# Performance work log

Measured on AMD Instinct MI355X. Metric: run time of the kernel, lower is better.

## Reference

```python
import jax, jax.numpy as jnp
import numpy as np

DT = 0.1
NUM_STEPS = 10
THRESHOLD = 0.3


def setup_inputs() -> dict:
    key = jax.random.key(0)
    k1, k2, k3 = jax.random.split(key, 3)
    B, T, D = 8, 4096, 1024
    L, O = 3, 4
    x = jax.random.normal(k1, (B, T, D), dtype=jnp.float32)
    # nn.Linear(dim, O, bias=False) weights per level, stacked: (L, O, D)
    W = jax.random.normal(k2, (L, O, D), dtype=jnp.float32) / np.sqrt(D)
    # omegas init: randn*0.1 + freq_scales[min(i,2)], freq_scales=[4.0,2.0,0.6]
    freq = jnp.array([4.0, 2.0, 0.6], dtype=jnp.float32)[:, None]
    omegas = jax.random.normal(k3, (L, O), dtype=jnp.float32) * 0.1 + freq
    # coupling strengths: 1.0 + i*0.5
    Ks = 1.0 + 0.5 * jnp.arange(L, dtype=jnp.float32)
    return {"x": x, "W": W, "omegas": omegas, "Ks": Ks}


def reference(x, W, omegas, Ks):
    B, T, D = x.shape
    L, O, _ = W.shape
    two_pi = 2.0 * jnp.pi

    # per-level projection: (L, B, T, O)
    proj = jnp.einsum('btd,lod->lbto', x, W)
    # initial phases from adjacent oscillator ratio
    phases = jnp.arctan2(proj, jnp.roll(proj, 1, axis=-1) + 1e-8) % two_pi

    om = omegas[:, None, None, :]      # (L,1,1,O)
    K = Ks[:, None, None, None]        # (L,1,1,1)

    def step(ph, _):
        # mean phase over time dim per oscillator (circular mean)
        mean_phase = jnp.arctan2(jnp.sin(ph).mean(axis=2, keepdims=True),
                                 jnp.cos(ph).mean(axis=2, keepdims=True))
        coupling = K * jnp.sin(mean_phase - ph) / T
        return (ph + DT * (om + coupling)) % two_pi, None

    phases, _ = jax.lax.scan(step, phases, None, length=NUM_STEPS)

    s = jnp.sin(phases)
    c = jnp.cos(phases)
    # global coherence: |mean_t exp(i*phi)| averaged over oscillators -> (B, L)
    level_coherences = jnp.sqrt(s.mean(axis=2) ** 2 + c.mean(axis=2) ** 2).mean(-1).T

    # sliding window-of-3 coherence along T -> (L, B, T-2)
    ms = (s[:, :, :-2] + s[:, :, 1:-1] + s[:, :, 2:]) / 3.0
    mc = (c[:, :, :-2] + c[:, :, 1:-1] + c[:, :, 2:]) / 3.0
    coh = jnp.sqrt(ms ** 2 + mc ** 2).mean(-1)
    # local-minimum dip detection: boundary at coherence index i+1 (i in 1..T-5)
    cond = (coh[..., 1:-1] < coh[..., :-2] - THRESHOLD) & \
           (coh[..., 1:-1] < coh[..., 2:] - THRESHOLD)      # (L, B, T-4)
    boundary_mask = jnp.pad(cond, ((0, 0), (0, 0), (2, 0)))   # (L, B, T-2)

    return phases, level_coherences, boundary_mask
```

## Files before the change

kernel.cpp:

```cpp
#include <hip/hip_runtime.h>
#include <math.h>

#define NB 8
#define NT 4096
#define ND 1024
#define NL 3
#define NO 4
#define NLO 12
#define TWO_PI_D 6.283185307179586476925286766559
#define DT_D 0.1
#define NSTEPS 10
#define THRESH_D 0.3

#define XPAD 132

__global__ __launch_bounds__(256) void k_wprep(const float* __restrict__ W,
                                               double* __restrict__ wsW)
{
    int i = blockIdx.x * 256 + threadIdx.x;
    if (i < NLO * ND) wsW[i] = (double)W[i];
}

__global__ __launch_bounds__(256, 2) void k_proj(
    const float* __restrict__ x, const double* __restrict__ wsW,
    double* __restrict__ ws_ph, double* __restrict__ ws_s,
    double* __restrict__ ws_c)
{
    __shared__ float  xl[64 * XPAD];
    __shared__ double wl[NLO * 128];
    __shared__ double red[4 * 16 * 4 * 13];

    const int tid = threadIdx.x;
    const int rowslot = tid & 15;
    const int seg = tid >> 4;
    const long row0 = (long)blockIdx.x * 64;

    double acc[4][NLO];
#pragma unroll
    for (int j = 0; j < 4; ++j)
#pragma unroll
        for (int lo = 0; lo < NLO; ++lo) acc[j][lo] = 0.0;

    for (int c = 0; c < ND / 128; ++c) {
#pragma unroll
        for (int p = 0; p < 8; ++p) {
            int id = p * 256 + tid;
            int r = id >> 5, col = id & 31;
            float4 v = *reinterpret_cast<const float4*>(
                x + (row0 + r) * ND + c * 128 + col * 4);
            *reinterpret_cast<float4*>(&xl[r * XPAD + col * 4]) = v;
        }
#pragma unroll
        for (int p = 0; p < 3; ++p) {
            int id = p * 256 + tid;
            int lo = id >> 6, dc = id & 63;
            double2 v = *reinterpret_cast<const double2*>(
                wsW + lo * ND + c * 128 + dc * 2);
            *reinterpret_cast<double2*>(&wl[lo * 128 + dc * 2]) = v;
        }
        __syncthreads();

        const int d0 = seg * 8;
        float xs[4][8];
#pragma unroll
        for (int j = 0; j < 4; ++j) {
            const float* xr = &xl[(rowslot * 4 + j) * XPAD + d0];
            float4 a = *reinterpret_cast<const float4*>(xr);
            float4 b = *reinterpret_cast<const float4*>(xr + 4);
            xs[j][0] = a.x; xs[j][1] = a.y; xs[j][2] = a.z; xs[j][3] = a.w;
            xs[j][4] = b.x; xs[j][5] = b.y; xs[j][6] = b.z; xs[j][7] = b.w;
        }
#pragma unroll
        for (int dp = 0; dp < 4; ++dp) {
            double2 wv[NLO];
#pragma unroll
            for (int lo = 0; lo < NLO; ++lo)
                wv[lo] = *reinterpret_cast<const double2*>(
                    &wl[lo * 128 + d0 + dp * 2]);
#pragma unroll
            for (int j = 0; j < 4; ++j) {
                double x0 = (double)xs[j][2 * dp];
                double x1 = (double)xs[j][2 * dp + 1];
#pragma unroll
                for (int lo = 0; lo < NLO; ++lo)
                    acc[j][lo] = fma(x1, wv[lo].y, fma(x0, wv[lo].x, acc[j][lo]));
            }
        }
        __syncthreads();
    }

#pragma unroll
    for (int j = 0; j < 4; ++j)
#pragma unroll
        for (int lo = 0; lo < NLO; ++lo) {
            double v = acc[j][lo];
            v += __shfl_xor(v, 16, 64);
            v += __shfl_xor(v, 32, 64);
            acc[j][lo] = v;
        }
    const int wv_ = tid >> 6;
    if ((tid & 63) < 16) {
#pragma unroll
        for (int j = 0; j < 4; ++j)
#pragma unroll
            for (int lo = 0; lo < NLO; ++lo)
                red[((wv_ * 16 + rowslot) * 4 + j) * 13 + lo] = acc[j][lo];
    }
    __syncthreads();

    if (tid < 64) {
        const int rs = tid >> 2, j = tid & 3;
        double proj[NLO];
#pragma unroll
        for (int lo = 0; lo < NLO; ++lo)
            proj[lo] = (red[((rs) * 4 + j) * 13 + lo] +
                        red[((16 + rs) * 4 + j) * 13 + lo]) +
                       (red[((32 + rs) * 4 + j) * 13 + lo] +
                        red[((48 + rs) * 4 + j) * 13 + lo]);
        const long row = row0 + tid;
        const int b = (int)(row >> 12);
        const int t = (int)(row & (NT - 1));
#pragma unroll
        for (int l = 0; l < NL; ++l)
#pragma unroll
            for (int o = 0; o < NO; ++o) {
                double y = proj[l * NO + o];
                double xx = proj[l * NO + ((o + 3) & 3)] + 1e-8;
                double ph = atan2(y, xx);
                if (ph < 0.0) ph += TWO_PI_D;
                double r2 = sqrt(y * y + xx * xx);
                double s, cc;
                if (r2 > 0.0) { s = y / r2; cc = xx / r2; } else { s = 0.0; cc = 1.0; }
                long idx = ((long)((l * NB + b) * NO + o)) * NT + t;
                ws_ph[idx] = ph; ws_s[idx] = s; ws_c[idx] = cc;
            }
    }
}

#define B_THREADS 512
#define B_ELEMS (NT / B_THREADS)

__global__ __launch_bounds__(B_THREADS) void k_kuramoto(
    const float* __restrict__ omegas, const float* __restrict__ Ks,
    double* __restrict__ ws_ph, double* __restrict__ ws_s,
    double* __restrict__ ws_c, double* __restrict__ ws_r,
    float* __restrict__ out_ph)
{
    const int g = blockIdx.x;
    const int l = g >> 5;
    const int b = (g >> 2) & 7;
    const int o = g & 3;
    const double om = (double)omegas[l * NO + o];
    const double Kv = (double)Ks[l];
    const int tid = threadIdx.x;
    const int wid = tid >> 6;
    const int lane = tid & 63;
    __shared__ double lds[18];

    double ph[B_ELEMS], s[B_ELEMS], c[B_ELEMS];
#pragma unroll
    for (int k = 0; k < B_ELEMS; ++k) {
        long idx = (long)g * NT + tid + k * B_THREADS;
        ph[k] = ws_ph[idx]; s[k] = ws_s[idx]; c[k] = ws_c[idx];
    }

    for (int step = 0; step < NSTEPS; ++step) {
        double ts = 0.0, tc = 0.0;
#pragma unroll
        for (int k = 0; k < B_ELEMS; ++k) { ts += s[k]; tc += c[k]; }
#pragma unroll
        for (int off = 32; off > 0; off >>= 1) {
            ts += __shfl_down(ts, off);
            tc += __shfl_down(tc, off);
        }
        if (lane == 0) { lds[wid] = ts; lds[8 + wid] = tc; }
        __syncthreads();
        if (tid == 0) {
            double S = 0.0, C = 0.0;
#pragma unroll
            for (int w = 0; w < 8; ++w) { S += lds[w]; C += lds[8 + w]; }
            double mean = atan2(S / (double)NT, C / (double)NT);
            double sm, cm; sincos(mean, &sm, &cm);
            lds[16] = sm; lds[17] = cm;
        }
        __syncthreads();
        const double sm = lds[16], cm = lds[17];
#pragma unroll
        for (int k = 0; k < B_ELEMS; ++k) {
            double sv = sm * c[k] - cm * s[k];
            double d = DT_D * (om + Kv * sv / (double)NT);
            double val = ph[k] + d;
            if (val >= TWO_PI_D) val -= TWO_PI_D;
            if (val < 0.0) val += TWO_PI_D;
            ph[k] = val;
            double z = d * d;
            double sd = d * fma(z, fma(z, fma(z, fma(z, 1.0 / 362880.0,
                          -1.0 / 5040.0), 1.0 / 120.0), -1.0 / 6.0), 1.0);
            double cd = fma(z, fma(z, fma(z, fma(z, 1.0 / 40320.0,
                          -1.0 / 720.0), 1.0 / 24.0), -0.5), 1.0);
            double sn = fma(s[k], cd, c[k] * sd);
            double cn = fma(c[k], cd, -(s[k] * sd));
            s[k] = sn; c[k] = cn;
        }
        __syncthreads();
    }
    {
        double ts = 0.0, tc = 0.0;
#pragma unroll
        for (int k = 0; k < B_ELEMS; ++k) { ts += s[k]; tc += c[k]; }
#pragma unroll
        for (int off = 32; off > 0; off >>= 1) {
            ts += __shfl_down(ts, off);
            tc += __shfl_down(tc, off);
        }
        if (lane == 0) { lds[wid] = ts; lds[8 + wid] = tc; }
        __syncthreads();
        if (tid == 0) {
            double S = 0.0, C = 0.0;
#pragma unroll
            for (int w = 0; w < 8; ++w) { S += lds[w]; C += lds[8 + w]; }
            double Sm = S / (double)NT, Cm = C / (double)NT;
            ws_r[g] = sqrt(Sm * Sm + Cm * Cm);
        }
    }
#pragma unroll
    for (int k = 0; k < B_ELEMS; ++k) {
        int t = tid + k * B_THREADS;
        long idx = (long)g * NT + t;
        ws_s[idx] = s[k]; ws_c[idx] = c[k];
        out_ph[((long)(l * NB + b) * NT + t) * NO + o] = (float)ph[k];
    }
}

__global__ __launch_bounds__(256) void k_mask(
    const double* __restrict__ ws_s, const double* __restrict__ ws_c,
    float* __restrict__ out_mask)
{
    const int bid = blockIdx.x;
    const int lb = bid >> 4;
    const int t0 = ((bid & 15) << 8) + threadIdx.x;
    float* mrow = out_mask + (long)lb * (NT - 2);
    if ((bid & 15) == 0 && threadIdx.x < 2) mrow[threadIdx.x] = 0.0f;
    if (t0 >= NT - 4) return;
    double q[3] = {0.0, 0.0, 0.0};
#pragma unroll
    for (int o = 0; o < NO; ++o) {
        const double* ps = ws_s + ((long)lb * NO + o) * NT + t0;
        const double* pc = ws_c + ((long)lb * NO + o) * NT + t0;
        double sv[5], cv[5];
#pragma unroll
        for (int j = 0; j < 5; ++j) { sv[j] = ps[j]; cv[j] = pc[j]; }
#pragma unroll
        for (int j = 0; j < 3; ++j) {
            double ms = ((sv[j] + sv[j + 1]) + sv[j + 2]) / 3.0;
            double mc = ((cv[j] + cv[j + 1]) + cv[j + 2]) / 3.0;
            q[j] += sqrt(ms * ms + mc * mc);
        }
    }
    double coh0 = q[0] / 4.0, coh1 = q[1] / 4.0, coh2 = q[2] / 4.0;
    bool cond = (coh1 < coh0 - THRESH_D) && (coh1 < coh2 - THRESH_D);
    mrow[2 + t0] = cond ? 1.0f : 0.0f;
}

__global__ void k_level(const double* __restrict__ ws_r, float* __restrict__ out_lvl)
{
    const int tid = threadIdx.x;
    if (tid < NB * NL) {
        const int b = tid / NL, l = tid % NL;
        const double* r = ws_r + (long)(l * NB + b) * NO;
        double m = (((r[0] + r[1]) + r[2]) + r[3]) / 4.0;
        out_lvl[tid] = (float)m;
    }
}

extern "C" void kernel_launch(void* const* d_in, const int* in_sizes, int n_in,
                              void* d_out, int out_size, void* d_ws, size_t ws_size,
                              hipStream_t stream)
{
    const float* x      = (const float*)d_in[0];
    const float* W      = (const float*)d_in[1];
    const float* omegas = (const float*)d_in[2];
    const float* Ks     = (const float*)d_in[3];
    float* out = (float*)d_out;

    double* wsW   = (double*)d_ws;
    double* ws_ph = wsW + NLO * ND;
    double* ws_s  = ws_ph + (long)NLO * NB * NT;
    double* ws_c  = ws_s + (long)NLO * NB * NT;
    double* ws_r  = ws_c + (long)NLO * NB * NT;

    float* out_ph   = out;
    float* out_lvl  = out + 393216;
    float* out_mask = out + 393240;

    k_wprep<<<(NLO * ND + 255) / 256, 256, 0, stream>>>(W, wsW);
    k_proj<<<NB * NT / 64, 256, 0, stream>>>(x, wsW, ws_ph, ws_s, ws_c);
    k_kuramoto<<<NL * NB * NO, B_THREADS, 0, stream>>>(omegas, Ks, ws_ph, ws_s, ws_c, ws_r, out_ph);
    k_mask<<<24 * 16, 256, 0, stream>>>(ws_s, ws_c, out_mask);
    k_level<<<1, 64, 0, stream>>>(ws_r, out_lvl);
}
```

Baseline: 79.75 us.

## Rework projection to per-row direct loads and simplify Kuramoto phase-rotation math

The projection kernel drops LDS staging of x and W. Each thread now owns one row and a 256-wide slice of D, reading x and the double weights straight from global memory into 32 doubles of registers, with a cross-wave reduction through shared memory afterwards. The Kuramoto step replaces atan2+sincos with a normalisation of (S,C). It also replaces the per-element Taylor polynomial for sin/cos of the phase increment with a precomputed sincos(dt*omega) plus a first-order correction in the small coupling term. The first-order correction is an approximation that drops terms of order eps squared, and the new projection relies on cache hits for the weights and raises register pressure.

```diff
diff --git a/kernel.cpp b/kernel.cpp
--- a/kernel.cpp
+++ b/kernel.cpp
@@ -12,8 +12,6 @@
 #define NSTEPS 10
 #define THRESH_D 0.3
 
-#define XPAD 132
-
 __global__ __launch_bounds__(256) void k_wprep(const float* __restrict__ W,
                                                double* __restrict__ wsW)
 {
@@ -21,105 +19,63 @@
     if (i < NLO * ND) wsW[i] = (double)W[i];
 }
 
-__global__ __launch_bounds__(256, 2) void k_proj(
+__global__ __launch_bounds__(256) void k_proj(
     const float* __restrict__ x, const double* __restrict__ wsW,
     double* __restrict__ ws_ph, double* __restrict__ ws_s,
     double* __restrict__ ws_c)
 {
-    __shared__ float  xl[64 * XPAD];
-    __shared__ double wl[NLO * 128];
-    __shared__ double red[4 * 16 * 4 * 13];
-
+    __shared__ double red[4 * 64 * 13];
     const int tid = threadIdx.x;
-    const int rowslot = tid & 15;
-    const int seg = tid >> 4;
-    const long row0 = (long)blockIdx.x * 64;
-
-    double acc[4][NLO];
-#pragma unroll
-    for (int j = 0; j < 4; ++j)
-#pragma unroll
-        for (int lo = 0; lo < NLO; ++lo) acc[j][lo] = 0.0;
-
-    for (int c = 0; c < ND / 128; ++c) {
-#pragma unroll
-        for (int p = 0; p < 8; ++p) {
-            int id = p * 256 + tid;
-            int r = id >> 5, col = id & 31;
-            float4 v = *reinterpret_cast<const float4*>(
-                x + (row0 + r) * ND + c * 128 + col * 4);
-            *reinterpret_cast<float4*>(&xl[r * XPAD + col * 4]) = v;
-        }
-#pragma unroll
-        for (int p = 0; p < 3; ++p) {
-            int id = p * 256 + tid;
-            int lo = id >> 6, dc = id & 63;
-            double2 v = *reinterpret_cast<const double2*>(
-                wsW + lo * ND + c * 128 + dc * 2);
-            *reinterpret_cast<double2*>(&wl[lo * 128 + dc * 2]) = v;
-        }
-        __syncthreads();
-
-        const int d0 = seg * 8;
-        float xs[4][8];
-#pragma unroll
-        for (int j = 0; j < 4; ++j) {
-            const float* xr = &xl[(rowslot * 4 + j) * XPAD + d0];
-            float4 a = *reinterpret_cast<const float4*>(xr);
-            float4 b = *reinterpret_cast<const float4*>(xr + 4);
-            xs[j][0] = a.x; xs[j][1] = a.y; xs[j][2] = a.z; xs[j][3] = a.w;
-            xs[j][4] = b.x; xs[j][5] = b.y; xs[j][6] = b.z; xs[j][7] = b.w;
-        }
-#pragma unroll
-        for (int dp = 0; dp < 4; ++dp) {
-            double2 wv[NLO];
-#pragma unroll
-            for (int lo = 0; lo < NLO; ++lo)
-                wv[lo] = *reinterpret_cast<const double2*>(
-                    &wl[lo * 128 + d0 + dp * 2]);
-#pragma unroll
-            for (int j = 0; j < 4; ++j) {
-                double x0 = (double)xs[j][2 * dp];
-                double x1 = (double)xs[j][2 * dp + 1];
-#pragma unroll
-                for (int lo = 0; lo < NLO; ++lo)
-                    acc[j][lo] = fma(x1, wv[lo].y, fma(x0, wv[lo].x, acc[j][lo]));
-            }
-        }
-        __syncthreads();
-    }
-
-#pragma unroll
-    for (int j = 0; j < 4; ++j)
+    const int lane = tid & 63;
+    const int wid = tid >> 6;
+    const long row = (long)blockIdx.x * 64 + lane;
+    const float* xr = x + row * ND + wid * 256;
+
+    double acc[NLO];
+#pragma unroll
+    for (int lo = 0; lo < NLO; ++lo) acc[lo] = 0.0;
+
+    for (int it = 0; it < 8; ++it) {
+        float4 f[8];
+#pragma unroll
+        for (int q = 0; q < 8; ++q)
+            f[q] = reinterpret_cast<const float4*>(xr + it * 32)[q];
+        double xd[32];
+#pragma unroll
+        for (int q = 0; q < 8; ++q) {
+            xd[q * 4 + 0] = (double)f[q].x;
+            xd[q * 4 + 1] = (double)f[q].y;
+            xd[q * 4 + 2] = (double)f[q].z;
+            xd[q * 4 + 3] = (double)f[q].w;
+        }
+        const double* wp = wsW + wid * 256 + it * 32;
 #pragma unroll
         for (int lo = 0; lo < NLO; ++lo) {
-            double v = acc[j][lo];
-            v += __shfl_xor(v, 16, 64);
-            v += __shfl_xor(v, 32, 64);
-            acc[j][lo] = v;
-        }
-    const int wv_ = tid >> 6;
-    if ((tid & 63) < 16) {
-#pragma unroll
-        for (int j = 0; j < 4; ++j)
-#pragma unroll
-            for (int lo = 0; lo < NLO; ++lo)
-                red[((wv_ * 16 + rowslot) * 4 + j) * 13 + lo] = acc[j][lo];
-    }
+            const double* w = wp + lo * ND;
+            double a = acc[lo];
+#pragma unroll
+            for (int q = 0; q < 32; ++q)
+                a = fma(xd[q], w[q], a);
+            acc[lo] = a;
+        }
+    }
+
+#pragma unroll
+    for (int lo = 0; lo < NLO; ++lo)
+        red[(wid * 64 + lane) * 13 + lo] = acc[lo];
     __syncthreads();
 
     if (tid < 64) {
-        const int rs = tid >> 2, j = tid & 3;
         double proj[NLO];
 #pragma unroll
         for (int lo = 0; lo < NLO; ++lo)
-            proj[lo] = (red[((rs) * 4 + j) * 13 + lo] +
-                        red[((16 + rs) * 4 + j) * 13 + lo]) +
-                       (red[((32 + rs) * 4 + j) * 13 + lo] +
-                        red[((48 + rs) * 4 + j) * 13 + lo]);
-        const long row = row0 + tid;
-        const int b = (int)(row >> 12);
-        const int t = (int)(row & (NT - 1));
+            proj[lo] = (red[(0 * 64 + tid) * 13 + lo] +
+                        red[(1 * 64 + tid) * 13 + lo]) +
+                       (red[(2 * 64 + tid) * 13 + lo] +
+                        red[(3 * 64 + tid) * 13 + lo]);
+        const long r = (long)blockIdx.x * 64 + tid;
+        const int b = (int)(r >> 12);
+        const int t = (int)(r & (NT - 1));
 #pragma unroll
         for (int l = 0; l < NL; ++l)
 #pragma unroll
@@ -152,6 +108,9 @@
     const int o = g & 3;
     const double om = (double)omegas[l * NO + o];
     const double Kv = (double)Ks[l];
+    const double dtom = DT_D * om;
+    const double cKT = DT_D * Kv / (double)NT;
+    double sA, cA; sincos(dtom, &sA, &cA);
     const int tid = threadIdx.x;
     const int wid = tid >> 6;
     const int lane = tid & 63;
@@ -179,8 +138,9 @@
             double S = 0.0, C = 0.0;
 #pragma unroll
             for (int w = 0; w < 8; ++w) { S += lds[w]; C += lds[8 + w]; }
-            double mean = atan2(S / (double)NT, C / (double)NT);
-            double sm, cm; sincos(mean, &sm, &cm);
+            double r2 = sqrt(S * S + C * C);
+            double sm, cm;
+            if (r2 > 0.0) { sm = S / r2; cm = C / r2; } else { sm = 0.0; cm = 1.0; }
             lds[16] = sm; lds[17] = cm;
         }
         __syncthreads();
@@ -188,16 +148,13 @@
 #pragma unroll
         for (int k = 0; k < B_ELEMS; ++k) {
             double sv = sm * c[k] - cm * s[k];
-            double d = DT_D * (om + Kv * sv / (double)NT);
-            double val = ph[k] + d;
+            double eps = cKT * sv;
+            double val = ph[k] + (dtom + eps);
             if (val >= TWO_PI_D) val -= TWO_PI_D;
             if (val < 0.0) val += TWO_PI_D;
             ph[k] = val;
-            double z = d * d;
-            double sd = d * fma(z, fma(z, fma(z, fma(z, 1.0 / 362880.0,
-                          -1.0 / 5040.0), 1.0 / 120.0), -1.0 / 6.0), 1.0);
-            double cd = fma(z, fma(z, fma(z, fma(z, 1.0 / 40320.0,
-                          -1.0 / 720.0), 1.0 / 24.0), -0.5), 1.0);
+            double sd = fma(cA, eps, sA);
+            double cd = fma(-sA, eps, cA);
             double sn = fma(s[k], cd, c[k] * sd);
             double cn = fma(c[k], cd, -(s[k] * sd));
             s[k] = sn; c[k] = cn;
```

After: 153.1 us. 1.92x slower.
